# Optimization experiments

Measured on AMD Instinct MI355X. Metric: run time of the kernel, lower is better.

Reference implementation:

```python
import jax, jax.numpy as jnp
import numpy as np

K = 3        # patch size (size=(3,3))
DIL = 1      # dilation
EPS = 1e-8


def _unfold(x, k=K, d=DIL):
    """im2col identical to torch.nn.Unfold(kernel_size=k, dilation=d).
    x: [N, C, H, W] -> [N, C*k*k, L], channel-major then (kh, kw) ordering."""
    N, C, H, W = x.shape
    Ho = H - d * (k - 1)
    Wo = W - d * (k - 1)
    rows = []
    for i in range(k):
        cols = [x[:, :, i * d:i * d + Ho, j * d:j * d + Wo] for j in range(k)]
        rows.append(jnp.stack(cols, axis=2))  # [N, C, k, Ho, Wo]
    patches = jnp.stack(rows, axis=2)         # [N, C, k, k, Ho, Wo]
    return patches.reshape(N, C * k * k, Ho * Wo)


def setup_inputs() -> dict:
    key = jax.random.key(0)
    k1, k2 = jax.random.split(key)
    x = jax.random.normal(k1, (1, 256, 96, 96), dtype=jnp.float32)
    style = jax.random.normal(k2, (1, 256, 96, 96), dtype=jnp.float32)
    return {"x": x, "style": style}


def reference(x, style):
    # Patches of input and style feature maps: [B, D, L] with D = C*3*3.
    ip = _unfold(x)       # [B, D, Li]
    sp = _unfold(style)   # [B, D, Ls]  (precomputed in __init__ in the torch module)

    # Normalized cross-correlation between every input patch and every style patch.
    ipn = ip / (jnp.linalg.norm(ip, axis=1, keepdims=True) + EPS)
    spn = sp / (jnp.linalg.norm(sp, axis=1, keepdims=True) + EPS)
    sim = jnp.einsum('bdi,bdj->bij', ipn, spn)  # [B, Li, Ls]

    # Nearest style patch for each input patch (Champandard patch matching).
    idx = jnp.argmax(sim, axis=2)                                  # [B, Li]
    matched = jnp.take_along_axis(sp, idx[:, None, :], axis=2)     # [B, D, Li]

    # MSE between input patches and their best-matching style patches.
    return jnp.mean((ip - matched) ** 2)
```

## Files before the change

kernel.cpp:

```cpp
#include <hip/hip_runtime.h>

#define CCH   256
#define HH    96
#define WW    96
#define HO    94
#define LL    8836
#define DD    2304
#define LPAD  8960

#define BM2   256
#define NT2   35
#define NPH   36
#define ASLB  16384
#define BBASEB 65536

typedef unsigned char u8;
typedef unsigned long long u64;

using i32x4 = __attribute__((ext_vector_type(4))) int;

#define OFF_BQ    20643840ull
#define OFF_RNB   41287680ull
#define OFF_N2B   41323520ull
#define OFF_W2X   41359360ull
#define OFF_QSA   41395200ull
#define OFF_QSB   41431040ull
#define OFF_COLS  41466880ull
#define OFF_SAF   41502720ull
#define OFF_P2    41538560ull
#define OFF_PM    41612288ull
#define OFF_BEST  41686016ull

__device__ __forceinline__ void gload16(const void* g, void* l) {
    __builtin_amdgcn_global_load_lds(
        (const __attribute__((address_space(1))) unsigned int*)g,
        (__attribute__((address_space(3))) unsigned int*)l,
        16, 0, 0);
}

__global__ __launch_bounds__(256) void k_chan_stats(const float* __restrict__ st,
                                                    const float* __restrict__ x,
                                                    float* __restrict__ P2,
                                                    float* __restrict__ PM) {
    int p = blockIdx.x * 256 + threadIdx.x;
    if (p >= 2 * HH * WW) return;
    const float* img = (p < HH * WW) ? st : x;
    int pp = (p < HH * WW) ? p : p - HH * WW;
    float s = 0.f, m = 0.f;
#pragma unroll 4
    for (int c = 0; c < CCH; ++c) {
        float v = img[c * (HH * WW) + pp];
        s += v * v;
        m = fmaxf(m, fabsf(v));
    }
    P2[p] = s;
    PM[p] = m;
}

__global__ __launch_bounds__(256) void k_win(const float* __restrict__ P2,
                                             const float* __restrict__ PM,
                                             float* __restrict__ rnB,
                                             float* __restrict__ n2B,
                                             float* __restrict__ win2x,
                                             float* __restrict__ qsA,
                                             float* __restrict__ qsB,
                                             float* __restrict__ colS,
                                             float* __restrict__ sAf) {
    int i = blockIdx.x * 256 + threadIdx.x;
    if (i >= LL) return;
    int y = i / HO, xc = i % HO;
    float ss = 0.f, sx = 0.f, ms = 0.f, mx = 0.f;
#pragma unroll
    for (int kh = 0; kh < 3; ++kh)
#pragma unroll
        for (int kw = 0; kw < 3; ++kw) {
            int off = (y + kh) * WW + xc + kw;
            ss += P2[off];
            sx += P2[HH * WW + off];
            ms = fmaxf(ms, PM[off]);
            mx = fmaxf(mx, PM[HH * WW + off]);
        }
    float rn = 1.f / (sqrtf(ss) + 1e-8f);
    float msc = fmaxf(ms, 1e-30f), mxc = fmaxf(mx, 1e-30f);
    rnB[i] = rn;
    n2B[i] = ss;
    win2x[i] = sx;
    qsA[i] = 127.f / mxc;
    qsB[i] = 127.f / msc;
    colS[i] = rn * msc * (1.f / 127.f);
    sAf[i] = mxc * (1.f / 127.f);
}

__global__ __launch_bounds__(256) void k_pack(const float* __restrict__ x,
                                              const float* __restrict__ st,
                                              const float* __restrict__ qsA,
                                              const float* __restrict__ qsB,
                                              u8* __restrict__ Aq,
                                              u8* __restrict__ Bq) {
    int row = blockIdx.x;
    bool isB = row >= LPAD;
    int i = isB ? row - LPAD : row;
    u8* dst = (isB ? Bq : Aq) + (size_t)i * DD + threadIdx.x * 9;
    if (i >= LL) {
#pragma unroll
        for (int k = 0; k < 9; ++k) dst[k] = 0;
        return;
    }
    int y = i / HO, xc = i % HO;
    const float* src = isB ? st : x;
    float scale = isB ? qsB[i] : qsA[i];
    const float* base = src + (size_t)threadIdx.x * (HH * WW) + y * WW + xc;
#pragma unroll
    for (int kh = 0; kh < 3; ++kh)
#pragma unroll
        for (int kw = 0; kw < 3; ++kw) {
            int q = (int)rintf(base[kh * WW + kw] * scale);
            dst[kh * 3 + kw] = (u8)q;
        }
}

__global__ __launch_bounds__(512, 2) void k_gemm2(const u8* __restrict__ A,
                                                  const u8* __restrict__ Bm,
                                                  const float* __restrict__ colS,
                                                  u64* __restrict__ best) {
    extern __shared__ __align__(16) u8 lds[];

    const int t = threadIdx.x;
    const int wid = t >> 6, lane = t & 63;
    const int wr = wid >> 2, wc = wid & 3;
    const int l15 = lane & 15, l4 = lane >> 4;

    const int nwg = NT2 * NT2;
    const int q = nwg >> 3, r = nwg & 7;
    const int bid = blockIdx.x;
    const int xcd = bid & 7, loc = bid >> 3;
    const int swz = ((xcd < r) ? xcd * (q + 1) : r * (q + 1) + (xcd - r) * q) + loc;
    const int it = swz / NT2, jt = swz % NT2;

    const int gsrc = (t & 3) ^ ((t >> 3) & 3);
    const u8* pA0 = A  + (size_t)(it * BM2 + (t >> 2)) * DD + gsrc * 16;
    const u8* pB0 = Bm + (size_t)(jt * BM2 + (t >> 2)) * DD + gsrc * 16;

    const int sp16 = (l4 ^ ((l15 >> 1) & 3)) * 16;
    int aoff[8], boff[4];
#pragma unroll
    for (int mi = 0; mi < 8; ++mi)
        aoff[mi] = (wr * 128 + mi * 16 + l15) * 64 + sp16;
#pragma unroll
    for (int ni = 0; ni < 4; ++ni)
        boff[ni] = BBASEB + (wc * 64 + ni * 16 + l15) * 64 + sp16;

    i32x4 acc[8][4];
#pragma unroll
    for (int mi = 0; mi < 8; ++mi)
#pragma unroll
        for (int ni = 0; ni < 4; ++ni)
            acc[mi][ni] = (i32x4){0, 0, 0, 0};

#define PSTAGE(S)                                                            \
    do {                                                                     \
        const u8* sa = pA0 + (size_t)(S) * 64;                               \
        const u8* sb = pB0 + (size_t)(S) * 64;                               \
        gload16(sa,          lds + (S) * ASLB + t * 16);                     \
        gload16(sa + 294912, lds + (S) * ASLB + 8192 + t * 16);              \
        gload16(sb,          lds + BBASEB + (S) * ASLB + t * 16);            \
        gload16(sb + 294912, lds + BBASEB + (S) * ASLB + 8192 + t * 16);     \
    } while (0)
    PSTAGE(0); PSTAGE(1); PSTAGE(2);
#undef PSTAGE
    asm volatile("s_waitcnt vmcnt(8)" ::: "memory");
    __builtin_amdgcn_sched_barrier(0);
    __builtin_amdgcn_s_barrier();

    i32x4 af03[4], af47[4], bfr[4];

#define SUBA(U)                                                              \
    {                                                                        \
        _Pragma("unroll")                                                    \
        for (int ni = 0; ni < 4; ++ni)                                       \
            bfr[ni] = *(const i32x4*)(lds + (U) * ASLB + boff[ni]);          \
        _Pragma("unroll")                                                    \
        for (int mi = 0; mi < 4; ++mi)                                       \
            af03[mi] = *(const i32x4*)(lds + (U) * ASLB + aoff[mi]);         \
        {                                                                    \
            const int ss = (kb + (U) + 3 > NPH - 1) ? (NPH - 1) : (kb + (U) + 3); \
            const u8* sa = pA0 + (size_t)ss * 64;                            \
            u8* da = lds + (((U) + 3) & 3) * ASLB + t * 16;                  \
            gload16(sa,          da);                                        \
            gload16(sa + 294912, da + 8192);                                 \
        }                                                                    \
        __builtin_amdgcn_s_barrier();                                        \
        asm volatile("s_waitcnt lgkmcnt(0)" ::: "memory");                   \
        __builtin_amdgcn_sched_barrier(0);                                   \
        __builtin_amdgcn_s_setprio(1);                                       \
        _Pragma("unroll")                                                    \
        for (int mi = 0; mi < 4; ++mi)                                       \
            _Pragma("unroll")                                                \
            for (int ni = 0; ni < 4; ++ni)                                   \
                acc[mi][ni] = __builtin_amdgcn_mfma_i32_16x16x64_i8(         \
                    af03[mi], bfr[ni], acc[mi][ni], 0, 0, 0);                \
        __builtin_amdgcn_s_setprio(0);                                       \
        __builtin_amdgcn_s_barrier();                                        \
    }

#define SUBB(U)                                                              \
    {                                                                        \
        _Pragma("unroll")                                                    \
        for (int mi = 0; mi < 4; ++mi)                                       \
            af47[mi] = *(const i32x4*)(lds + (U) * ASLB + aoff[4 + mi]);     \
        {                                                                    \
            const int ss = (kb + (U) + 3 > NPH - 1) ? (NPH - 1) : (kb + (U) + 3); \
            const u8* sb = pB0 + (size_t)ss * 64;                            \
            u8* db = lds + BBASEB + (((U) + 3) & 3) * ASLB + t * 16;         \
            gload16(sb,          db);                                        \
            gload16(sb + 294912, db + 8192);                                 \
        }                                                                    \
        asm volatile("s_waitcnt vmcnt(8)" ::: "memory");                     \
        __builtin_amdgcn_sched_barrier(0);                                   \
        __builtin_amdgcn_s_barrier();                                        \
        asm volatile("s_waitcnt lgkmcnt(0)" ::: "memory");                   \
        __builtin_amdgcn_sched_barrier(0);                                   \
        __builtin_amdgcn_s_setprio(1);                                       \
        _Pragma("unroll")                                                    \
        for (int mi = 0; mi < 4; ++mi)                                       \
            _Pragma("unroll")                                                \
            for (int ni = 0; ni < 4; ++ni)                                   \
                acc[4 + mi][ni] = __builtin_amdgcn_mfma_i32_16x16x64_i8(     \
                    af47[mi], bfr[ni], acc[4 + mi][ni], 0, 0, 0);            \
        __builtin_amdgcn_s_setprio(0);                                       \
        __builtin_amdgcn_s_barrier();                                        \
    }

    for (int kt = 0; kt < NPH / 4; ++kt) {
        const int kb = kt * 4;
        SUBA(0) SUBB(0)
        SUBA(1) SUBB(1)
        SUBA(2) SUBB(2)
        SUBA(3) SUBB(3)
    }
#undef SUBA
#undef SUBB

    const int jbase = jt * BM2 + wc * 64 + l15;
    float cs[4];
#pragma unroll
    for (int ni = 0; ni < 4; ++ni) {
        int j = jbase + ni * 16;
        cs[ni] = colS[j < LL ? j : 0];
    }
#pragma unroll
    for (int mi = 0; mi < 8; ++mi) {
#pragma unroll
        for (int rr = 0; rr < 4; ++rr) {
            float bv = -3.4e38f;
            int bj = 0x7FFFFFFF;
#pragma unroll
            for (int ni = 0; ni < 4; ++ni) {
                int j = jbase + ni * 16;
                float v = (float)acc[mi][ni][rr] * cs[ni];
                if (j < LL && (v > bv || (v == bv && j < bj))) { bv = v; bj = j; }
            }
#pragma unroll
            for (int m = 1; m < 16; m <<= 1) {
                float ov = __shfl_xor(bv, m, 64);
                int oj = __shfl_xor(bj, m, 64);
                if (ov > bv || (ov == bv && oj < bj)) { bv = ov; bj = oj; }
            }
            if (l15 == 0) {
                int i = it * BM2 + wr * 128 + mi * 16 + l4 * 4 + rr;
                if (i < LL) {
                    unsigned u = __float_as_uint(bv);
                    unsigned s = (bv < 0.f) ? ~u : (u | 0x80000000u);
                    u64 packed = ((u64)s << 32) | (unsigned)(~(unsigned)bj);
                    atomicMax(&best[i], packed);
                }
            }
        }
    }
}

__global__ __launch_bounds__(256) void k_final(const u64* __restrict__ best,
                                               const float* __restrict__ rnB,
                                               const float* __restrict__ n2B,
                                               const float* __restrict__ win2x,
                                               const float* __restrict__ sAf,
                                               float* __restrict__ out) {
    int i = blockIdx.x * 256 + threadIdx.x;
    float contrib = 0.f;
    if (i < LL) {
        u64 p = best[i];
        unsigned s = (unsigned)(p >> 32);
        unsigned ub = (s & 0x80000000u) ? (s & 0x7FFFFFFFu) : ~s;
        float bv = __uint_as_float(ub);
        int j = (int)(~(unsigned)(p & 0xFFFFFFFFull));
        float dot = (bv * sAf[i]) / rnB[j];
        contrib = win2x[i] + n2B[j] - 2.f * dot;
    }
    float sred = contrib;
#pragma unroll
    for (int o = 32; o > 0; o >>= 1) sred += __shfl_down(sred, o, 64);
    __shared__ float red[4];
    if ((threadIdx.x & 63) == 0) red[threadIdx.x >> 6] = sred;
    __syncthreads();
    if (threadIdx.x == 0) {
        float tot = red[0] + red[1] + red[2] + red[3];
        atomicAdd(out, tot * (1.0f / ((float)DD * (float)LL)));
    }
}

extern "C" void kernel_launch(void* const* d_in, const int* in_sizes, int n_in,
                              void* d_out, int out_size, void* d_ws, size_t ws_size,
                              hipStream_t stream) {
    const float* x  = (const float*)d_in[0];
    const float* st = (const float*)d_in[1];
    char* ws = (char*)d_ws;

    u8* Aq       = (u8*)ws;
    u8* Bq       = (u8*)(ws + OFF_BQ);
    float* rnB   = (float*)(ws + OFF_RNB);
    float* n2B   = (float*)(ws + OFF_N2B);
    float* win2x = (float*)(ws + OFF_W2X);
    float* qsA   = (float*)(ws + OFF_QSA);
    float* qsB   = (float*)(ws + OFF_QSB);
    float* colS  = (float*)(ws + OFF_COLS);
    float* sAf   = (float*)(ws + OFF_SAF);
    float* P2    = (float*)(ws + OFF_P2);
    float* PM    = (float*)(ws + OFF_PM);
    u64* best    = (u64*)(ws + OFF_BEST);
    float* out   = (float*)d_out;

    hipFuncSetAttribute((const void*)k_gemm2,
                        hipFuncAttributeMaxDynamicSharedMemorySize, 131072);

    hipMemsetAsync(best, 0, (size_t)LL * 8, stream);
    hipMemsetAsync(out, 0, sizeof(float), stream);

    k_chan_stats<<<dim3(72), dim3(256), 0, stream>>>(st, x, P2, PM);
    k_win<<<dim3(35), dim3(256), 0, stream>>>(P2, PM, rnB, n2B, win2x, qsA, qsB, colS, sAf);
    k_pack<<<dim3(2 * LPAD), dim3(256), 0, stream>>>(x, st, qsA, qsB, Aq, Bq);
    k_gemm2<<<dim3(NT2 * NT2), dim3(512), 131072, stream>>>(Aq, Bq, colS, best);
    k_final<<<dim3(35), dim3(256), 0, stream>>>(best, rnB, n2B, win2x, sAf, out);
}
```

Before: 400.3 us.

## Restructure int8 GEMM main loop into a two-stage double buffer with interleaved fragment loads

Replaces the four-deep LDS ring, which loaded A and B in separate half-steps, with a two-slot double buffer. Each K-step now prefetches the full A and B tiles for the next step and issues all fragment reads at once. A partial lgkmcnt wait lets the first MFMAs start while later A fragments are still arriving from LDS. Dynamic LDS per workgroup is halved, which could allow two workgroups per CU. The cost is only one stage of global-load lookahead, more live fragment registers, and one harmless over-read past the last K-step.

Result: slower. 424.6 us (+6.1%).

```diff
diff --git a/kernel.cpp b/kernel.cpp
--- a/kernel.cpp
+++ b/kernel.cpp
@@ -11,8 +11,8 @@
 #define BM2   256
 #define NT2   35
 #define NPH   36
-#define ASLB  16384
-#define BBASEB 65536
+#define SLOTB 32768
+#define ROWS2 294912
 
 typedef unsigned char u8;
 typedef unsigned long long u64;
@@ -138,8 +138,10 @@
     const int it = swz / NT2, jt = swz % NT2;
 
     const int gsrc = (t & 3) ^ ((t >> 3) & 3);
-    const u8* pA0 = A  + (size_t)(it * BM2 + (t >> 2)) * DD + gsrc * 16;
-    const u8* pB0 = Bm + (size_t)(jt * BM2 + (t >> 2)) * DD + gsrc * 16;
+    const int laneG = (t >> 2) * DD + gsrc * 16;
+    const u8* pAblk = A  + (size_t)(it * BM2) * DD;
+    const u8* pBblk = Bm + (size_t)(jt * BM2) * DD;
+    u8* ldsT = lds + t * 16;
 
     const int sp16 = (l4 ^ ((l15 >> 1) & 3)) * 16;
     int aoff[8], boff[4];
@@ -148,7 +150,7 @@
         aoff[mi] = (wr * 128 + mi * 16 + l15) * 64 + sp16;
 #pragma unroll
     for (int ni = 0; ni < 4; ++ni)
-        boff[ni] = BBASEB + (wc * 64 + ni * 16 + l15) * 64 + sp16;
+        boff[ni] = 16384 + (wc * 64 + ni * 16 + l15) * 64 + sp16;
 
     i32x4 acc[8][4];
 #pragma unroll
@@ -157,89 +159,83 @@
         for (int ni = 0; ni < 4; ++ni)
             acc[mi][ni] = (i32x4){0, 0, 0, 0};
 
-#define PSTAGE(S)                                                            \
-    do {                                                                     \
-        const u8* sa = pA0 + (size_t)(S) * 64;                               \
-        const u8* sb = pB0 + (size_t)(S) * 64;                               \
-        gload16(sa,          lds + (S) * ASLB + t * 16);                     \
-        gload16(sa + 294912, lds + (S) * ASLB + 8192 + t * 16);              \
-        gload16(sb,          lds + BBASEB + (S) * ASLB + t * 16);            \
-        gload16(sb + 294912, lds + BBASEB + (S) * ASLB + 8192 + t * 16);     \
-    } while (0)
-    PSTAGE(0); PSTAGE(1); PSTAGE(2);
-#undef PSTAGE
-    asm volatile("s_waitcnt vmcnt(8)" ::: "memory");
-    __builtin_amdgcn_sched_barrier(0);
-    __builtin_amdgcn_s_barrier();
-
-    i32x4 af03[4], af47[4], bfr[4];
-
-#define SUBA(U)                                                              \
+    gload16(pAblk + laneG,          ldsT);
+    gload16(pAblk + laneG + ROWS2,  ldsT + 8192);
+    gload16(pBblk + laneG,          ldsT + 16384);
+    gload16(pBblk + laneG + ROWS2,  ldsT + 24576);
+
+#define BODY(SREL, SL)                                                       \
     {                                                                        \
-        _Pragma("unroll")                                                    \
-        for (int ni = 0; ni < 4; ++ni)                                       \
-            bfr[ni] = *(const i32x4*)(lds + (U) * ASLB + boff[ni]);          \
-        _Pragma("unroll")                                                    \
-        for (int mi = 0; mi < 4; ++mi)                                       \
-            af03[mi] = *(const i32x4*)(lds + (U) * ASLB + aoff[mi]);         \
-        {                                                                    \
-            const int ss = (kb + (U) + 3 > NPH - 1) ? (NPH - 1) : (kb + (U) + 3); \
-            const u8* sa = pA0 + (size_t)ss * 64;                            \
-            u8* da = lds + (((U) + 3) & 3) * ASLB + t * 16;                  \
-            gload16(sa,          da);                                        \
-            gload16(sa + 294912, da + 8192);                                 \
-        }                                                                    \
+        const u8* pAs = pAblk + (size_t)(s4 + (SREL) + 1) * 64;              \
+        const u8* pBs = pBblk + (size_t)(s4 + (SREL) + 1) * 64;              \
+        u8* d = ldsT + (1 - (SL)) * SLOTB;                                   \
+        gload16(pAs + laneG,         d);                                     \
+        gload16(pAs + laneG + ROWS2, d + 8192);                              \
+        gload16(pBs + laneG,         d + 16384);                             \
+        gload16(pBs + laneG + ROWS2, d + 24576);                             \
+        asm volatile("s_waitcnt vmcnt(4)" ::: "memory");                     \
+        __builtin_amdgcn_sched_barrier(0);                                   \
         __builtin_amdgcn_s_barrier();                                        \
+        i32x4 af0, af1, af2, af3, af4, af5, af6, af7, bf0, bf1, bf2, bf3;    \
+        af0 = *(const i32x4*)(lds + (SL) * SLOTB + aoff[0]);                 \
+        af1 = *(const i32x4*)(lds + (SL) * SLOTB + aoff[1]);                 \
+        bf0 = *(const i32x4*)(lds + (SL) * SLOTB + boff[0]);                 \
+        bf1 = *(const i32x4*)(lds + (SL) * SLOTB + boff[1]);                 \
+        bf2 = *(const i32x4*)(lds + (SL) * SLOTB + boff[2]);                 \
+        bf3 = *(const i32x4*)(lds + (SL) * SLOTB + boff[3]);                 \
+        __builtin_amdgcn_sched_barrier(0);                                   \
+        af2 = *(const i32x4*)(lds + (SL) * SLOTB + aoff[2]);                 \
+        af3 = *(const i32x4*)(lds + (SL) * SLOTB + aoff[3]);                 \
+        af4 = *(const i32x4*)(lds + (SL) * SLOTB + aoff[4]);                 \
+        af5 = *(const i32x4*)(lds + (SL) * SLOTB + aoff[5]);                 \
+        af6 = *(const i32x4*)(lds + (SL) * SLOTB + aoff[6]);                 \
+        af7 = *(const i32x4*)(lds + (SL) * SLOTB + aoff[7]);                 \
+        asm volatile("s_waitcnt lgkmcnt(6)" ::: "memory");                   \
+        __builtin_amdgcn_sched_barrier(0);                                   \
+        __builtin_amdgcn_s_setprio(1);                                       \
+        acc[0][0] = __builtin_amdgcn_mfma_i32_16x16x64_i8(af0, bf0, acc[0][0], 0, 0, 0); \
+        acc[0][1] = __builtin_amdgcn_mfma_i32_16x16x64_i8(af0, bf1, acc[0][1], 0, 0, 0); \
+        acc[0][2] = __builtin_amdgcn_mfma_i32_16x16x64_i8(af0, bf2, acc[0][2], 0, 0, 0); \
+        acc[0][3] = __builtin_amdgcn_mfma_i32_16x16x64_i8(af0, bf3, acc[0][3], 0, 0, 0); \
+        acc[1][0] = __builtin_amdgcn_mfma_i32_16x16x64_i8(af1, bf0, acc[1][0], 0, 0, 0); \
+        acc[1][1] = __builtin_amdgcn_mfma_i32_16x16x64_i8(af1, bf1, acc[1][1], 0, 0, 0); \
+        acc[1][2] = __builtin_amdgcn_mfma_i32_16x16x64_i8(af1, bf2, acc[1][2], 0, 0, 0); \
+        acc[1][3] = __builtin_amdgcn_mfma_i32_16x16x64_i8(af1, bf3, acc[1][3], 0, 0, 0); \
         asm volatile("s_waitcnt lgkmcnt(0)" ::: "memory");                   \
         __builtin_amdgcn_sched_barrier(0);                                   \
-        __builtin_amdgcn_s_setprio(1);                                       \
-        _Pragma("unroll")                                                    \
-        for (int mi = 0; mi < 4; ++mi)                                       \
-            _Pragma("unroll")                                                \
-            for (int ni = 0; ni < 4; ++ni)                                   \
-                acc[mi][ni] = __builtin_amdgcn_mfma_i32_16x16x64_i8(         \
-                    af03[mi], bfr[ni], acc[mi][ni], 0, 0, 0);                \
+        acc[2][0] = __builtin_amdgcn_mfma_i32_16x16x64_i8(af2, bf0, acc[2][0], 0, 0, 0); \
+        acc[2][1] = __builtin_amdgcn_mfma_i32_16x16x64_i8(af2, bf1, acc[2][1], 0, 0, 0); \
+        acc[2][2] = __builtin_amdgcn_mfma_i32_16x16x64_i8(af2, bf2, acc[2][2], 0, 0, 0); \
+        acc[2][3] = __builtin_amdgcn_mfma_i32_16x16x64_i8(af2, bf3, acc[2][3], 0, 0, 0); \
+        acc[3][0] = __builtin_amdgcn_mfma_i32_16x16x64_i8(af3, bf0, acc[3][0], 0, 0, 0); \
+        acc[3][1] = __builtin_amdgcn_mfma_i32_16x16x64_i8(af3, bf1, acc[3][1], 0, 0, 0); \
+        acc[3][2] = __builtin_amdgcn_mfma_i32_16x16x64_i8(af3, bf2, acc[3][2], 0, 0, 0); \
+        acc[3][3] = __builtin_amdgcn_mfma_i32_16x16x64_i8(af3, bf3, acc[3][3], 0, 0, 0); \
+        acc[4][0] = __builtin_amdgcn_mfma_i32_16x16x64_i8(af4, bf0, acc[4][0], 0, 0, 0); \
+        acc[4][1] = __builtin_amdgcn_mfma_i32_16x16x64_i8(af4, bf1, acc[4][1], 0, 0, 0); \
+        acc[4][2] = __builtin_amdgcn_mfma_i32_16x16x64_i8(af4, bf2, acc[4][2], 0, 0, 0); \
+        acc[4][3] = __builtin_amdgcn_mfma_i32_16x16x64_i8(af4, bf3, acc[4][3], 0, 0, 0); \
+        acc[5][0] = __builtin_amdgcn_mfma_i32_16x16x64_i8(af5, bf0, acc[5][0], 0, 0, 0); \
+        acc[5][1] = __builtin_amdgcn_mfma_i32_16x16x64_i8(af5, bf1, acc[5][1], 0, 0, 0); \
+        acc[5][2] = __builtin_amdgcn_mfma_i32_16x16x64_i8(af5, bf2, acc[5][2], 0, 0, 0); \
+        acc[5][3] = __builtin_amdgcn_mfma_i32_16x16x64_i8(af5, bf3, acc[5][3], 0, 0, 0); \
+        acc[6][0] = __builtin_amdgcn_mfma_i32_16x16x64_i8(af6, bf0, acc[6][0], 0, 0, 0); \
+        acc[6][1] = __builtin_amdgcn_mfma_i32_16x16x64_i8(af6, bf1, acc[6][1], 0, 0, 0); \
+        acc[6][2] = __builtin_amdgcn_mfma_i32_16x16x64_i8(af6, bf2, acc[6][2], 0, 0, 0); \
+        acc[6][3] = __builtin_amdgcn_mfma_i32_16x16x64_i8(af6, bf3, acc[6][3], 0, 0, 0); \
+        acc[7][0] = __builtin_amdgcn_mfma_i32_16x16x64_i8(af7, bf0, acc[7][0], 0, 0, 0); \
+        acc[7][1] = __builtin_amdgcn_mfma_i32_16x16x64_i8(af7, bf1, acc[7][1], 0, 0, 0); \
+        acc[7][2] = __builtin_amdgcn_mfma_i32_16x16x64_i8(af7, bf2, acc[7][2], 0, 0, 0); \
+        acc[7][3] = __builtin_amdgcn_mfma_i32_16x16x64_i8(af7, bf3, acc[7][3], 0, 0, 0); \
         __builtin_amdgcn_s_setprio(0);                                       \
         __builtin_amdgcn_s_barrier();                                        \
     }
 
-#define SUBB(U)                                                              \
-    {                                                                        \
-        _Pragma("unroll")                                                    \
-        for (int mi = 0; mi < 4; ++mi)                                       \
-            af47[mi] = *(const i32x4*)(lds + (U) * ASLB + aoff[4 + mi]);     \
-        {                                                                    \
-            const int ss = (kb + (U) + 3 > NPH - 1) ? (NPH - 1) : (kb + (U) + 3); \
-            const u8* sb = pB0 + (size_t)ss * 64;                            \
-            u8* db = lds + BBASEB + (((U) + 3) & 3) * ASLB + t * 16;         \
-            gload16(sb,          db);                                        \
-            gload16(sb + 294912, db + 8192);                                 \
-        }                                                                    \
-        asm volatile("s_waitcnt vmcnt(8)" ::: "memory");                     \
-        __builtin_amdgcn_sched_barrier(0);                                   \
-        __builtin_amdgcn_s_barrier();                                        \
-        asm volatile("s_waitcnt lgkmcnt(0)" ::: "memory");                   \
-        __builtin_amdgcn_sched_barrier(0);                                   \
-        __builtin_amdgcn_s_setprio(1);                                       \
-        _Pragma("unroll")                                                    \
-        for (int mi = 0; mi < 4; ++mi)                                       \
-            _Pragma("unroll")                                                \
-            for (int ni = 0; ni < 4; ++ni)                                   \
-                acc[4 + mi][ni] = __builtin_amdgcn_mfma_i32_16x16x64_i8(     \
-                    af47[mi], bfr[ni], acc[4 + mi][ni], 0, 0, 0);            \
-        __builtin_amdgcn_s_setprio(0);                                       \
-        __builtin_amdgcn_s_barrier();                                        \
-    }
-
-    for (int kt = 0; kt < NPH / 4; ++kt) {
-        const int kb = kt * 4;
-        SUBA(0) SUBB(0)
-        SUBA(1) SUBB(1)
-        SUBA(2) SUBB(2)
-        SUBA(3) SUBB(3)
-    }
-#undef SUBA
-#undef SUBB
+    for (int s4 = 0; s4 < NPH; s4 += 2) {
+        BODY(0, 0)
+        BODY(1, 1)
+    }
+#undef BODY
 
     const int jbase = jt * BM2 + wc * 64 + l15;
     float cs[4];
@@ -330,7 +326,7 @@
     float* out   = (float*)d_out;
 
     hipFuncSetAttribute((const void*)k_gemm2,
-                        hipFuncAttributeMaxDynamicSharedMemorySize, 131072);
+                        hipFuncAttributeMaxDynamicSharedMemorySize, 65536);
 
     hipMemsetAsync(best, 0, (size_t)LL * 8, stream);
     hipMemsetAsync(out, 0, sizeof(float), stream);
@@ -338,6 +334,6 @@
     k_chan_stats<<<dim3(72), dim3(256), 0, stream>>>(st, x, P2, PM);
     k_win<<<dim3(35), dim3(256), 0, stream>>>(P2, PM, rnB, n2B, win2x, qsA, qsB, colS, sAf);
     k_pack<<<dim3(2 * LPAD), dim3(256), 0, stream>>>(x, st, qsA, qsB, Aq, Bq);
-    k_gemm2<<<dim3(NT2 * NT2), dim3(512), 131072, stream>>>(Aq, Bq, colS, best);
+    k_gemm2<<<dim3(NT2 * NT2), dim3(512), 65536, stream>>>(Aq, Bq, colS, best);
     k_final<<<dim3(35), dim3(256), 0, stream>>>(best, rnB, n2B, win2x, sAf, out);
 }
```

## Stage packed int8 patch rows in LDS and store with 16-byte writes

Applied to the files above, without the earlier changes.

k_pack now handles 47 output positions of one image row per block, one (kh,kw) pair per thread, looping over channels. Each thread's input reads are coalesced across threads, and its results go into LDS. The packed rows are then written to global memory with 16-byte vector stores instead of scattered 9-byte byte stores. Padding rows are cleared by memsets instead of kernel threads. This uses about 108 KB of LDS per block, which limits occupancy, and only 376 blocks are launched.

Result: no change. 400.0 us (-0.1%).

```diff
diff --git a/kernel.cpp b/kernel.cpp
--- a/kernel.cpp
+++ b/kernel.cpp
@@ -91,32 +91,42 @@
     sAf[i] = mxc * (1.f / 127.f);
 }
 
-__global__ __launch_bounds__(256) void k_pack(const float* __restrict__ x,
+__global__ __launch_bounds__(512) void k_pack(const float* __restrict__ x,
                                               const float* __restrict__ st,
                                               const float* __restrict__ qsA,
                                               const float* __restrict__ qsB,
                                               u8* __restrict__ Aq,
                                               u8* __restrict__ Bq) {
-    int row = blockIdx.x;
-    bool isB = row >= LPAD;
-    int i = isB ? row - LPAD : row;
-    u8* dst = (isB ? Bq : Aq) + (size_t)i * DD + threadIdx.x * 9;
-    if (i >= LL) {
-#pragma unroll
-        for (int k = 0; k < 9; ++k) dst[k] = 0;
-        return;
-    }
-    int y = i / HO, xc = i % HO;
-    const float* src = isB ? st : x;
-    float scale = isB ? qsB[i] : qsA[i];
-    const float* base = src + (size_t)threadIdx.x * (HH * WW) + y * WW + xc;
-#pragma unroll
-    for (int kh = 0; kh < 3; ++kh)
-#pragma unroll
-        for (int kw = 0; kw < 3; ++kw) {
-            int q = (int)rintf(base[kh * WW + kw] * scale);
-            dst[kh * 3 + kw] = (u8)q;
+    extern __shared__ u8 plds[];
+
+    const int b = blockIdx.x;
+    const int side = b & 1;
+    const int half = (b >> 1) & 1;
+    const int y = b >> 2;
+    const int xc0 = half * 47;
+
+    const float* src = side ? st : x;
+    const float* qs  = side ? qsB : qsA;
+    u8* dst = (side ? Bq : Aq) + (size_t)(y * HO + xc0) * DD;
+
+    const int t = threadIdx.x;
+    if (t < 47 * 9) {
+        const int il = t / 9, k = t - il * 9;
+        const int kh = k / 3, kw = k - kh * 3;
+        const int i = y * HO + xc0 + il;
+        const float scale = qs[i];
+        const float* sp = src + (y + kh) * WW + (xc0 + il + kw);
+        u8* lp = plds + il * DD + k;
+#pragma unroll 8
+        for (int c = 0; c < CCH; ++c) {
+            int qv = (int)rintf(sp[c * (HH * WW)] * scale);
+            lp[c * 9] = (u8)qv;
         }
+    }
+    __syncthreads();
+    for (int idx = t; idx < 6768; idx += 512) {
+        *(i32x4*)(dst + idx * 16) = *(const i32x4*)(plds + idx * 16);
+    }
 }
 
 __global__ __launch_bounds__(512, 2) void k_gemm2(const u8* __restrict__ A,
@@ -212,7 +222,7 @@
             const int ss = (kb + (U) + 3 > NPH - 1) ? (NPH - 1) : (kb + (U) + 3); \
             const u8* sb = pB0 + (size_t)ss * 64;                            \
             u8* db = lds + BBASEB + (((U) + 3) & 3) * ASLB + t * 16;         \
-            gload16(sb,          db);                                        \
+            gload16(sb,          db);                                       \
             gload16(sb + 294912, db + 8192);                                 \
         }                                                                    \
         asm volatile("s_waitcnt vmcnt(8)" ::: "memory");                     \
@@ -331,13 +341,17 @@
 
     hipFuncSetAttribute((const void*)k_gemm2,
                         hipFuncAttributeMaxDynamicSharedMemorySize, 131072);
+    hipFuncSetAttribute((const void*)k_pack,
+                        hipFuncAttributeMaxDynamicSharedMemorySize, 110592);
 
     hipMemsetAsync(best, 0, (size_t)LL * 8, stream);
     hipMemsetAsync(out, 0, sizeof(float), stream);
+    hipMemsetAsync(Aq + (size_t)LL * DD, 0, (size_t)(LPAD - LL) * DD, stream);
+    hipMemsetAsync(Bq + (size_t)LL * DD, 0, (size_t)(LPAD - LL) * DD, stream);
 
     k_chan_stats<<<dim3(72), dim3(256), 0, stream>>>(st, x, P2, PM);
     k_win<<<dim3(35), dim3(256), 0, stream>>>(P2, PM, rnB, n2B, win2x, qsA, qsB, colS, sAf);
-    k_pack<<<dim3(2 * LPAD), dim3(256), 0, stream>>>(x, st, qsA, qsB, Aq, Bq);
+    k_pack<<<dim3(HO * 4), dim3(512), 108288, stream>>>(x, st, qsA, qsB, Aq, Bq);
     k_gemm2<<<dim3(NT2 * NT2), dim3(512), 131072, stream>>>(Aq, Bq, colS, best);
     k_final<<<dim3(35), dim3(256), 0, stream>>>(best, rnB, n2B, win2x, sAf, out);
 }
```
